# Kernel tuning notes

Hardware: AMD Instinct MI355X
Metric: run time of the kernel (lower is better)

## Reference

```python
import jax, jax.numpy as jnp
import numpy as np

H = 4          # no_heads
C_HIDDEN = 32  # per-head hidden dim


def setup_inputs() -> dict:
    key = jax.random.key(0)
    ks = jax.random.split(key, 11)
    B, S, C = 1, 256, 128
    sc = 1.0 / np.sqrt(C).astype(np.float32)
    return {
        "q_x": jax.random.normal(ks[0], (B, S, S, C), jnp.float32),
        "kv_x": jax.random.normal(ks[1], (B, S, S, C), jnp.float32),
        "bias1": jax.random.normal(ks[2], (B, 1, H, S, S), jnp.float32),
        "bias2": jax.random.normal(ks[3], (B, S, 1, 1, S), jnp.float32),
        "wq": jax.random.normal(ks[4], (C, C), jnp.float32) * sc,
        "wk": jax.random.normal(ks[5], (C, C), jnp.float32) * sc,
        "wv": jax.random.normal(ks[6], (C, C), jnp.float32) * sc,
        "wg": jax.random.normal(ks[7], (C, C), jnp.float32) * sc,
        "bg": jax.random.normal(ks[8], (C,), jnp.float32) * 0.02,
        "wo": jax.random.normal(ks[9], (C, C), jnp.float32) * sc,
        "bo": jax.random.normal(ks[10], (C,), jnp.float32) * 0.02,
    }


def reference(q_x, kv_x, bias1, bias2, wq, wk, wv, wg, bg, wo, bo):
    # Linear projections (torch Linear semantics: x @ W^T), no bias on q/k/v.
    def split_heads(x):  # ... Q (H C) -> ... H Q C
        *lead, Q, _ = x.shape
        return jnp.moveaxis(x.reshape(*lead, Q, H, C_HIDDEN), -2, -3)

    q = split_heads(jnp.einsum('...qi,oi->...qo', q_x, wq)) / np.sqrt(C_HIDDEN)
    k = split_heads(jnp.einsum('...ki,oi->...ko', kv_x, wk))
    v = split_heads(jnp.einsum('...ki,oi->...ko', kv_x, wv))

    # scores: [B, S, H, Q, K]
    a = jnp.einsum('bshqd,bshkd->bshqk', q, k)
    a = a + bias1 + bias2
    a = jax.nn.softmax(a, axis=-1)
    o = jnp.einsum('bshqk,bshkd->bshqd', a, v)
    o = jnp.moveaxis(o, -3, -2)  # ... H Q C -> ... Q H C

    # sigmoid gating
    g = jax.nn.sigmoid(jnp.einsum('...qi,oi->...qo', q_x, wg) + bg)
    *lead, Q, _ = g.shape
    g = g.reshape(*lead, Q, H, C_HIDDEN)
    o = o * g

    o = o.reshape(*lead, Q, H * C_HIDDEN)
    return jnp.einsum('...qi,oi->...qo', o, wo) + bo
```

## Files before the change

### kernel.cpp

```cpp
#include <hip/hip_runtime.h>
#include <math.h>

typedef _Float16 f16;
typedef _Float16 h4 __attribute__((ext_vector_type(4)));
typedef _Float16 h8 __attribute__((ext_vector_type(8)));
typedef float f32x4 __attribute__((ext_vector_type(4)));

#define QSCALE 0.17677669529663689f

__global__ __launch_bounds__(256) void proj_mfma(
    const float* __restrict__ q_x, const float* __restrict__ kv_x,
    const float* __restrict__ wq, const float* __restrict__ wk,
    const float* __restrict__ wv, const float* __restrict__ wg,
    const float* __restrict__ bg,
    f16* __restrict__ qb, f16* __restrict__ kb,
    f16* __restrict__ vbT, f16* __restrict__ gb)
{
    __shared__ char lds[65536];
    char* xl = lds;
    char* wl = lds + 32768;
    const int t = threadIdx.x;
    const int lane = t & 63, wave = t >> 6;
    const int wr = wave >> 1, wc = wave & 1;
    const int lo = lane & 15, hi = lane >> 4;
    const int phase = blockIdx.y;
    const int row0 = blockIdx.x * 128;
    const float* xsrc = phase ? kv_x : q_x;

    #pragma unroll
    for (int j = 0; j < 16; ++j) {
        int f = t + 256 * j;
        int row = f >> 5, c4 = f & 31;
        float4 v = *(const float4*)(xsrc + (size_t)(row0 + row) * 128 + c4 * 4);
        h4 hv = {(f16)v.x, (f16)v.y, (f16)v.z, (f16)v.w};
        *(h4*)(xl + row * 256 + (((c4 >> 1) ^ (row & 7)) << 4) + ((c4 & 1) << 3)) = hv;
    }

    for (int sub = 0; sub < 2; ++sub) {
        const int pid = phase * 2 + sub;
        const float* w = (pid == 0) ? wq : (pid == 1) ? wg : (pid == 2) ? wk : wv;
        __syncthreads();
        #pragma unroll
        for (int j = 0; j < 16; ++j) {
            int f = t + 256 * j;
            int row = f >> 5, c4 = f & 31;
            float4 v = *(const float4*)(w + (size_t)row * 128 + c4 * 4);
            h4 hv = {(f16)v.x, (f16)v.y, (f16)v.z, (f16)v.w};
            *(h4*)(wl + row * 256 + (((c4 >> 1) ^ (row & 7)) << 4) + ((c4 & 1) << 3)) = hv;
        }
        __syncthreads();

        f32x4 acc[4][4];
        #pragma unroll
        for (int m = 0; m < 4; ++m)
            #pragma unroll
            for (int n = 0; n < 4; ++n) acc[m][n] = (f32x4){0.f, 0.f, 0.f, 0.f};

        #pragma unroll
        for (int kk = 0; kk < 4; ++kk) {
            const int swz = ((hi + 4 * kk) ^ (lo & 7)) << 4;
            h8 af[4], bf[4];
            #pragma unroll
            for (int m = 0; m < 4; ++m)
                af[m] = *(const h8*)(xl + (lo + 16 * m + 64 * wr) * 256 + swz);
            #pragma unroll
            for (int n = 0; n < 4; ++n)
                bf[n] = *(const h8*)(wl + (lo + 16 * n + 64 * wc) * 256 + swz);
            #pragma unroll
            for (int m = 0; m < 4; ++m)
                #pragma unroll
                for (int n = 0; n < 4; ++n)
                    acc[m][n] = __builtin_amdgcn_mfma_f32_16x16x32_f16(af[m], bf[n], acc[m][n], 0, 0, 0);
        }

        #pragma unroll
        for (int n = 0; n < 4; ++n) {
            const int col = 64 * wc + 16 * n + lo;
            const float bgv = (pid == 1) ? bg[col] : 0.f;
            #pragma unroll
            for (int m = 0; m < 4; ++m) {
                if (pid == 3) {
                    int rg = row0 + 64 * wr + 16 * m + 4 * hi;
                    int sidx = rg >> 8, key = rg & 255;
                    int hh = col >> 5, dh = col & 31;
                    h4 hv = {(f16)acc[m][n][0], (f16)acc[m][n][1],
                             (f16)acc[m][n][2], (f16)acc[m][n][3]};
                    *(h4*)(vbT + (((size_t)sidx * 4 + hh) * 32 + dh) * 256 + key) = hv;
                } else {
                    f16* dst = (pid == 0) ? qb : (pid == 1) ? gb : kb;
                    #pragma unroll
                    for (int r = 0; r < 4; ++r) {
                        int rg = row0 + 64 * wr + 16 * m + 4 * hi + r;
                        float v = acc[m][n][r];
                        if (pid == 0) v *= QSCALE;
                        else if (pid == 1) v = 1.f / (1.f + __expf(-(v + bgv)));
                        dst[(size_t)rg * 128 + col] = (f16)v;
                    }
                }
            }
        }
    }
}

__global__ __launch_bounds__(256, 2) void attn_mfma(
    const f16* __restrict__ qb, const f16* __restrict__ kb,
    const f16* __restrict__ vbT, const f16* __restrict__ gb,
    const float* __restrict__ bias1, const float* __restrict__ bias2,
    f16* __restrict__ ob)
{
    extern __shared__ char smem[];
    char* klds = smem;
    char* vlds = smem + 16384;
    char* plds = smem + 32768;
    const int s = blockIdx.x, h = blockIdx.y;
    const int t = threadIdx.x, wave = t >> 6, lane = t & 63;
    const int lo = lane & 15, hi = lane >> 4;
    char* pw = plds + wave * 8192;
    const size_t rowbase = (size_t)s * 256;
    const f16* kslab = kb + rowbase * 128 + h * 32;
    const f16* vslab = vbT + ((size_t)s * 4 + h) * 32 * 256;
    const float* b1 = bias1 + (size_t)h * 65536;
    const float* b2 = bias2 + (size_t)s * 256;

    #pragma unroll
    for (int it = 0; it < 4; ++it) {
        int idx = t + 256 * it;
        int key = idx >> 2, c = idx & 3;
        h8 v = *(const h8*)(kslab + (size_t)key * 128 + c * 8);
        *(h8*)(klds + ((key >> 5) * 4 + c) * 512 + (key & 31) * 16) = v;
    }
    #pragma unroll
    for (int it = 0; it < 4; ++it) {
        int idx = t + 256 * it;
        int d = idx & 31, kc = idx >> 5;
        h8 v = *(const h8*)(vslab + (size_t)d * 256 + kc * 8);
        *(h8*)(vlds + kc * 512 + d * 16) = v;
    }
    __syncthreads();

    for (int pass = 0; pass < 2; ++pass) {
        const int q0 = pass * 128 + wave * 32;

        h8 qf[2];
        #pragma unroll
        for (int m = 0; m < 2; ++m)
            qf[m] = *(const h8*)(qb + (rowbase + q0 + 16 * m + lo) * 128 + h * 32 + 8 * hi);

        f32x4 O[2][2];
        float mrun[2][4], lrun[2][4];
        #pragma unroll
        for (int m = 0; m < 2; ++m) {
            #pragma unroll
            for (int n2 = 0; n2 < 2; ++n2) O[m][n2] = (f32x4){0.f, 0.f, 0.f, 0.f};
            #pragma unroll
            for (int r = 0; r < 4; ++r) { mrun[m][r] = -1e30f; lrun[m][r] = 0.f; }
        }

        #pragma unroll
        for (int ch = 0; ch < 2; ++ch) {
            f32x4 acc[2][8];
            #pragma unroll
            for (int m = 0; m < 2; ++m)
                #pragma unroll
                for (int nt = 0; nt < 8; ++nt) {
                    const float b2v = b2[ch * 128 + 16 * nt + lo];
                    #pragma unroll
                    for (int r = 0; r < 4; ++r)
                        acc[m][nt][r] = b1[(size_t)(q0 + 16 * m + 4 * hi + r) * 256
                                           + ch * 128 + 16 * nt + lo] + b2v;
                }
            #pragma unroll
            for (int nt = 0; nt < 8; ++nt) {
                const int ntg = ch * 8 + nt;
                h8 kf = *(const h8*)(klds + ((ntg >> 1) * 4 + hi) * 512
                                     + ((ntg & 1) * 16 + lo) * 16);
                #pragma unroll
                for (int m = 0; m < 2; ++m)
                    acc[m][nt] = __builtin_amdgcn_mfma_f32_16x16x32_f16(qf[m], kf, acc[m][nt], 0, 0, 0);
            }

            float scale[2][4];
            #pragma unroll
            for (int m = 0; m < 2; ++m)
                #pragma unroll
                for (int r = 0; r < 4; ++r) {
                    float mx = acc[m][0][r];
                    #pragma unroll
                    for (int nt = 1; nt < 8; ++nt) mx = fmaxf(mx, acc[m][nt][r]);
                    #pragma unroll
                    for (int w = 1; w < 16; w <<= 1) mx = fmaxf(mx, __shfl_xor(mx, w, 16));
                    const float mn = fmaxf(mrun[m][r], mx);
                    scale[m][r] = __expf(mrun[m][r] - mn);
                    mrun[m][r] = mn;
                    float sm = 0.f;
                    #pragma unroll
                    for (int nt = 0; nt < 8; ++nt) {
                        float p = __expf(acc[m][nt][r] - mn);
                        acc[m][nt][r] = p;
                        sm += p;
                    }
                    #pragma unroll
                    for (int w = 1; w < 16; w <<= 1) sm += __shfl_xor(sm, w, 16);
                    lrun[m][r] = lrun[m][r] * scale[m][r] + sm;
                }
            #pragma unroll
            for (int m = 0; m < 2; ++m)
                #pragma unroll
                for (int n2 = 0; n2 < 2; ++n2)
                    #pragma unroll
                    for (int r = 0; r < 4; ++r) O[m][n2][r] *= scale[m][r];

            #pragma unroll
            for (int m = 0; m < 2; ++m)
                #pragma unroll
                for (int nt = 0; nt < 8; ++nt)
                    #pragma unroll
                    for (int r = 0; r < 4; ++r) {
                        const int row = 16 * m + 4 * hi + r;
                        const int cs = ((2 * nt + (lo >> 3)) ^ ((4 * m + hi) << 1)) & 15;
                        *(f16*)(pw + row * 256 + cs * 16 + (lo & 7) * 2) = (f16)acc[m][nt][r];
                    }

            #pragma unroll
            for (int kt = 0; kt < 4; ++kt) {
                #pragma unroll
                for (int m = 0; m < 2; ++m) {
                    const int row = 16 * m + lo;
                    const int cs = ((4 * kt + hi) ^ ((4 * m + (lo >> 2)) << 1)) & 15;
                    h8 pa = *(const h8*)(pw + row * 256 + cs * 16);
                    #pragma unroll
                    for (int n2 = 0; n2 < 2; ++n2) {
                        h8 vf = *(const h8*)(vlds + (ch * 16 + 4 * kt + hi) * 512
                                             + (16 * n2 + lo) * 16);
                        O[m][n2] = __builtin_amdgcn_mfma_f32_16x16x32_f16(pa, vf, O[m][n2], 0, 0, 0);
                    }
                }
            }
        }

        #pragma unroll
        for (int m = 0; m < 2; ++m)
            #pragma unroll
            for (int r = 0; r < 4; ++r) {
                const float inv = 1.f / lrun[m][r];
                #pragma unroll
                for (int n2 = 0; n2 < 2; ++n2) {
                    size_t idx = (rowbase + q0 + 16 * m + 4 * hi + r) * 128
                                 + h * 32 + 16 * n2 + lo;
                    ob[idx] = (f16)(O[m][n2][r] * inv * (float)gb[idx]);
                }
            }
    }
}

__global__ __launch_bounds__(256) void out_mfma(
    const f16* __restrict__ ob, const float* __restrict__ wo,
    const float* __restrict__ bo, float* __restrict__ out)
{
    __shared__ char lds[65536];
    char* xl = lds;
    char* wl = lds + 32768;
    const int t = threadIdx.x;
    const int lane = t & 63, wave = t >> 6;
    const int wr = wave >> 1, wc = wave & 1;
    const int lo = lane & 15, hi = lane >> 4;
    const int row0 = blockIdx.x * 128;

    #pragma unroll
    for (int j = 0; j < 8; ++j) {
        int f = t + 256 * j;
        int row = f >> 4, c8 = f & 15;
        h8 v = *(const h8*)(ob + (size_t)(row0 + row) * 128 + c8 * 8);
        *(h8*)(xl + row * 256 + ((c8 ^ (row & 7)) << 4)) = v;
    }
    #pragma unroll
    for (int j = 0; j < 16; ++j) {
        int f = t + 256 * j;
        int row = f >> 5, c4 = f & 31;
        float4 v = *(const float4*)(wo + (size_t)row * 128 + c4 * 4);
        h4 hv = {(f16)v.x, (f16)v.y, (f16)v.z, (f16)v.w};
        *(h4*)(wl + row * 256 + (((c4 >> 1) ^ (row & 7)) << 4) + ((c4 & 1) << 3)) = hv;
    }
    __syncthreads();

    f32x4 acc[4][4];
    #pragma unroll
    for (int m = 0; m < 4; ++m)
        #pragma unroll
        for (int n = 0; n < 4; ++n) acc[m][n] = (f32x4){0.f, 0.f, 0.f, 0.f};

    #pragma unroll
    for (int kk = 0; kk < 4; ++kk) {
        const int swz = ((hi + 4 * kk) ^ (lo & 7)) << 4;
        h8 af[4], bf[4];
        #pragma unroll
        for (int m = 0; m < 4; ++m)
            af[m] = *(const h8*)(xl + (lo + 16 * m + 64 * wr) * 256 + swz);
        #pragma unroll
        for (int n = 0; n < 4; ++n)
            bf[n] = *(const h8*)(wl + (lo + 16 * n + 64 * wc) * 256 + swz);
        #pragma unroll
        for (int m = 0; m < 4; ++m)
            #pragma unroll
            for (int n = 0; n < 4; ++n)
                acc[m][n] = __builtin_amdgcn_mfma_f32_16x16x32_f16(af[m], bf[n], acc[m][n], 0, 0, 0);
    }

    #pragma unroll
    for (int n = 0; n < 4; ++n) {
        const int col = 64 * wc + 16 * n + lo;
        const float bov = bo[col];
        #pragma unroll
        for (int m = 0; m < 4; ++m)
            #pragma unroll
            for (int r = 0; r < 4; ++r)
                out[(size_t)(row0 + 64 * wr + 16 * m + 4 * hi + r) * 128 + col] = acc[m][n][r] + bov;
    }
}

extern "C" void kernel_launch(void* const* d_in, const int* in_sizes, int n_in,
                              void* d_out, int out_size, void* d_ws, size_t ws_size,
                              hipStream_t stream)
{
    const float* q_x   = (const float*)d_in[0];
    const float* kv_x  = (const float*)d_in[1];
    const float* bias1 = (const float*)d_in[2];
    const float* bias2 = (const float*)d_in[3];
    const float* wq    = (const float*)d_in[4];
    const float* wk    = (const float*)d_in[5];
    const float* wv    = (const float*)d_in[6];
    const float* wg    = (const float*)d_in[7];
    const float* bg    = (const float*)d_in[8];
    const float* wo    = (const float*)d_in[9];
    const float* bo    = (const float*)d_in[10];
    float* out = (float*)d_out;

    const size_t RC = (size_t)65536 * 128;
    f16* ws  = (f16*)d_ws;
    f16* qb  = ws;
    f16* kb  = ws + RC;
    f16* vbT = ws + 2 * RC;
    f16* gb  = ws + 3 * RC;
    f16* ob  = ws + 4 * RC;

    proj_mfma<<<dim3(512, 2), 256, 0, stream>>>(q_x, kv_x, wq, wk, wv, wg, bg, qb, kb, vbT, gb);
    attn_mfma<<<dim3(256, 4), 256, 65536, stream>>>(qb, kb, vbT, gb, bias1, bias2, ob);
    out_mfma<<<512, 256, 0, stream>>>(ob, wo, bo, out);
}
```

Measured before the change: 139.7 us.

## Read K and V fragments directly from global memory instead of LDS staging

The attention kernel stops staging the per-slab K and V tiles into shared memory and instead loads MFMA operand fragments straight from global (cache-resident) memory. This removes the prologue copy and block barrier and cuts LDS from 64KB to 32KB, which should allow more resident blocks per CU. The P-tile swizzle is also rewritten to key on row&7. The cost is repeated global/L2 loads of K and V by each wave and both passes, which adds memory latency inside the inner loop.

```diff
diff --git a/kernel.cpp b/kernel.cpp
--- a/kernel.cpp
+++ b/kernel.cpp
@@ -108,10 +108,7 @@
     const float* __restrict__ bias1, const float* __restrict__ bias2,
     f16* __restrict__ ob)
 {
-    extern __shared__ char smem[];
-    char* klds = smem;
-    char* vlds = smem + 16384;
-    char* plds = smem + 32768;
+    __shared__ char plds[32768];
     const int s = blockIdx.x, h = blockIdx.y;
     const int t = threadIdx.x, wave = t >> 6, lane = t & 63;
     const int lo = lane & 15, hi = lane >> 4;
@@ -122,22 +119,6 @@
     const float* b1 = bias1 + (size_t)h * 65536;
     const float* b2 = bias2 + (size_t)s * 256;
 
-    #pragma unroll
-    for (int it = 0; it < 4; ++it) {
-        int idx = t + 256 * it;
-        int key = idx >> 2, c = idx & 3;
-        h8 v = *(const h8*)(kslab + (size_t)key * 128 + c * 8);
-        *(h8*)(klds + ((key >> 5) * 4 + c) * 512 + (key & 31) * 16) = v;
-    }
-    #pragma unroll
-    for (int it = 0; it < 4; ++it) {
-        int idx = t + 256 * it;
-        int d = idx & 31, kc = idx >> 5;
-        h8 v = *(const h8*)(vslab + (size_t)d * 256 + kc * 8);
-        *(h8*)(vlds + kc * 512 + d * 16) = v;
-    }
-    __syncthreads();
-
     for (int pass = 0; pass < 2; ++pass) {
         const int q0 = pass * 128 + wave * 32;
 
@@ -171,9 +152,7 @@
                 }
             #pragma unroll
             for (int nt = 0; nt < 8; ++nt) {
-                const int ntg = ch * 8 + nt;
-                h8 kf = *(const h8*)(klds + ((ntg >> 1) * 4 + hi) * 512
-                                     + ((ntg & 1) * 16 + lo) * 16);
+                h8 kf = *(const h8*)(kslab + (size_t)(ch * 128 + 16 * nt + lo) * 128 + 8 * hi);
                 #pragma unroll
                 for (int m = 0; m < 2; ++m)
                     acc[m][nt] = __builtin_amdgcn_mfma_f32_16x16x32_f16(qf[m], kf, acc[m][nt], 0, 0, 0);
@@ -217,7 +196,7 @@
                     #pragma unroll
                     for (int r = 0; r < 4; ++r) {
                         const int row = 16 * m + 4 * hi + r;
-                        const int cs = ((2 * nt + (lo >> 3)) ^ ((4 * m + hi) << 1)) & 15;
+                        const int cs = ((2 * nt + (lo >> 3)) ^ ((row & 7) << 1)) & 15;
                         *(f16*)(pw + row * 256 + cs * 16 + (lo & 7) * 2) = (f16)acc[m][nt][r];
                     }
 
@@ -226,12 +205,12 @@
                 #pragma unroll
                 for (int m = 0; m < 2; ++m) {
                     const int row = 16 * m + lo;
-                    const int cs = ((4 * kt + hi) ^ ((4 * m + (lo >> 2)) << 1)) & 15;
+                    const int cs = ((4 * kt + hi) ^ ((row & 7) << 1)) & 15;
                     h8 pa = *(const h8*)(pw + row * 256 + cs * 16);
                     #pragma unroll
                     for (int n2 = 0; n2 < 2; ++n2) {
-                        h8 vf = *(const h8*)(vlds + (ch * 16 + 4 * kt + hi) * 512
-                                             + (16 * n2 + lo) * 16);
+                        h8 vf = *(const h8*)(vslab + (size_t)(16 * n2 + lo) * 256
+                                             + ch * 128 + 32 * kt + 8 * hi);
                         O[m][n2] = __builtin_amdgcn_mfma_f32_16x16x32_f16(pa, vf, O[m][n2], 0, 0, 0);
                     }
                 }
@@ -344,6 +323,6 @@
     f16* ob  = ws + 4 * RC;
 
     proj_mfma<<<dim3(512, 2), 256, 0, stream>>>(q_x, kv_x, wq, wk, wv, wg, bg, qb, kb, vbT, gb);
-    attn_mfma<<<dim3(256, 4), 256, 65536, stream>>>(qb, kb, vbT, gb, bias1, bias2, ob);
+    attn_mfma<<<dim3(256, 4), 256, 0, stream>>>(qb, kb, vbT, gb, bias1, bias2, ob);
     out_mfma<<<512, 256, 0, stream>>>(ob, wo, bo, out);
 }
```

Result: slower. 230.0 us (+64.6%).
